# Kernel tuning notes

Hardware: AMD Instinct MI355X
Metric: run time of the kernel (lower is better)

## Reference

```python
import jax, jax.numpy as jnp
import numpy as np

T = 4096        # sequence length
D = 128         # input feature dim
TRACE = 64      # trace_size
CONTEXT = 64    # context_size
HID = 64        # internal dense width (hardcoded 64 in module)
OUT = 128       # output_size
LN_EPS = 1e-6   # flax LayerNorm default epsilon


def setup_inputs() -> dict:
    key = jax.random.key(0)
    ks = jax.random.split(key, 12)

    def dense(k, fi, fo):
        return (jax.random.normal(k, (fi, fo), jnp.float32) / np.sqrt(fi).astype(np.float32))

    inp = {}
    inp["x"] = jax.random.normal(ks[0], (T, D), jnp.float32)
    inp["state"] = jnp.zeros((1, TRACE, CONTEXT), jnp.complex64)
    inp["start"] = jax.random.uniform(ks[1], (T,)) < 0.01  # sparse episode resets
    # deterministic FFM decay / frequency params (init_deterministic)
    inp["a"] = jnp.linspace(1e-6, 0.5, TRACE).astype(jnp.float32)
    inp["b"] = (2.0 * jnp.pi / jnp.linspace(1.0, 1000.0, CONTEXT)).astype(jnp.float32)
    inp["W1"] = dense(ks[2], D, HID);               inp["b1"] = jnp.zeros((HID,), jnp.float32)
    inp["W2"] = dense(ks[3], HID, 2 * TRACE);       inp["b2"] = jnp.zeros((2 * TRACE,), jnp.float32)
    inp["Wgi"] = dense(ks[4], 2 * TRACE, TRACE);    inp["bgi"] = jnp.zeros((TRACE,), jnp.float32)
    inp["Wp"] = dense(ks[5], 2 * TRACE, TRACE);     inp["bp"] = jnp.zeros((TRACE,), jnp.float32)
    inp["Wz"] = dense(ks[6], 2 * TRACE * CONTEXT, HID); inp["bz"] = jnp.zeros((HID,), jnp.float32)
    inp["Wgo"] = dense(ks[7], 2 * TRACE, HID);      inp["bgo"] = jnp.zeros((HID,), jnp.float32)
    inp["Ws"] = dense(ks[8], 2 * TRACE, HID);       inp["bs"] = jnp.zeros((HID,), jnp.float32)
    inp["W3"] = dense(ks[9], HID, HID);             inp["b3"] = jnp.zeros((HID,), jnp.float32)
    inp["W4"] = dense(ks[10], HID, OUT);            inp["b4"] = jnp.zeros((OUT,), jnp.float32)
    return inp


def _ffm_scan(scan_in, state0, start, a, b):
    # scan_in: (T, TRACE, CONTEXT) float, state0: (1, TRACE, CONTEXT) complex64
    t = scan_in.shape[0]
    timestep = jnp.ones((t + 1, 1, 1), dtype=jnp.int32)
    start_f = jnp.concatenate(
        [jnp.zeros((1, 1, 1), dtype=bool), start.reshape(t, 1, 1)], axis=0)
    xs = jnp.concatenate([state0, scan_in.astype(jnp.complex64)], axis=0)

    neg_a = -jnp.abs(a).reshape(1, TRACE, 1)
    b_r = b.reshape(1, 1, CONTEXT)
    ab = neg_a + 1j * b_r  # (1, TRACE, CONTEXT) complex

    def gamma(j):
        # j: (N,1,1) int -> (N, TRACE, CONTEXT) complex decay
        return jnp.exp(ab * j.astype(jnp.float32))

    def combine(carry, incoming):
        prev_start, s, i = carry
        st, xx, j = incoming
        keep = jnp.logical_not(st)
        s = s * keep
        j = j * keep.astype(j.dtype)
        new_s = s * gamma(j) + xx
        return (jnp.logical_or(st, prev_start), new_s, j + i)

    _, new_state, _ = jax.lax.associative_scan(
        combine, (start_f, xs, timestep), axis=0)
    return new_state[1:]  # (T, TRACE, CONTEXT) complex64


def _layernorm(x):
    mu = jnp.mean(x, axis=-1, keepdims=True)
    var = jnp.var(x, axis=-1, keepdims=True)
    return (x - mu) * jax.lax.rsqrt(var + LN_EPS)


def _forward(x, state, start, a, b, W1, b1, W2, b2, Wgi, bgi, Wp, bp,
             Wz, bz, Wgo, bgo, Ws, bs, W3, b3, W4, b4):
    h = jax.nn.relu(x @ W1 + b1)                 # (T, 64)
    h2 = h @ W2 + b2                             # (T, 2*TRACE)
    gate_in = jax.nn.sigmoid(h2 @ Wgi + bgi)     # (T, TRACE)
    pre = jax.nn.sigmoid(h2 @ Wp + bp)           # (T, TRACE)
    gated = pre * gate_in                        # (T, TRACE)
    scan_in = jnp.broadcast_to(gated[:, :, None], (gated.shape[0], TRACE, CONTEXT))
    state_seq = _ffm_scan(scan_in, state, start, a, b)  # (T, TRACE, CONTEXT) c64
    z_in = jnp.concatenate([jnp.real(state_seq), jnp.imag(state_seq)],
                           axis=-1).reshape(state_seq.shape[0], -1)
    z = z_in @ Wz + bz                           # (T, 64)
    gate_out = jax.nn.sigmoid(h2 @ Wgo + bgo)    # (T, 64)
    skip = h2 @ Ws + bs                          # (T, 64)
    out = _layernorm(z * gate_out) + skip * (1.0 - gate_out)
    out = jax.nn.relu(out @ W3 + b3)
    out = out @ W4 + b4                          # (T, OUT)
    return out, state_seq[-1:]


def reference(x, state, start, a, b, W1, b1, W2, b2, Wgi, bgi, Wp, bp,
              Wz, bz, Wgo, bgo, Ws, bs, W3, b3, W4, b4):
    return _forward(x, state, start, a, b, W1, b1, W2, b2, Wgi, bgi, Wp, bp,
                    Wz, bz, Wgo, bgo, Ws, bs, W3, b3, W4, b4)
```

## Files before the change

kernel.cpp:

```cpp
#include <hip/hip_runtime.h>
#include <math.h>

#define T_LEN 4096
#define D_IN 128
#define HID 64
#define KDIM 4096
#define K2   8192

#define OFF_GATED 0u
#define OFF_GO    262144u
#define OFF_SKIP  524288u
#define OFF_PART  786432u
#define OFF_FLAGS 2883584u
#define OFF_CHS   2887680u
#define OFF_WZT   2887744u
#define OFF_STBF  3149888u

typedef __attribute__((ext_vector_type(8))) short short8v;
typedef __attribute__((ext_vector_type(4))) float float4v;

__device__ __forceinline__ float sigm(float x){ return 1.f/(1.f+expf(-x)); }
__device__ __forceinline__ unsigned short f2bf(float x){
    unsigned int u = __float_as_uint(x);
    return (unsigned short)((u + 0x7FFFu + ((u >> 16) & 1u)) >> 16);
}

__global__ __launch_bounds__(512) void k_prep(
    const unsigned char* __restrict__ su8, const int* __restrict__ si32,
    int* __restrict__ flags, int* __restrict__ chunkStart,
    const float* __restrict__ Wz, unsigned short* __restrict__ wzt,
    const float* __restrict__ x,
    const float* __restrict__ W1, const float* __restrict__ b1,
    const float* __restrict__ W2, const float* __restrict__ b2,
    const float* __restrict__ Wgi, const float* __restrict__ bgi,
    const float* __restrict__ Wp,  const float* __restrict__ bp,
    const float* __restrict__ Wgo, const float* __restrict__ bgo,
    const float* __restrict__ Wsk, const float* __restrict__ bsk,
    float* __restrict__ gated, float* __restrict__ go, float* __restrict__ sk)
{
    const int bx = blockIdx.x;
    const int tid = threadIdx.x;

    if (bx == 0) {
        __shared__ int cnt;
        if (tid == 0) cnt = 0;
        __syncthreads();
        int local = 0;
        for (int i = tid; i < 4096; i += 512)
            if (i & 3) local += su8[i];
        if (local) atomicAdd(&cnt, local);
        __syncthreads();
        if (cnt > 0) {
            for (int i = tid; i < 4096; i += 512) flags[i] = su8[i] ? 1 : 0;
        } else {
            for (int i = tid; i < 4096; i += 512) flags[i] = si32[i] ? 1 : 0;
        }
        __syncthreads();
        if (tid < 64) {
            int any = 0;
#pragma unroll 8
            for (int j = 0; j < 64; ++j) any |= flags[tid * 64 + j];
            chunkStart[tid] = any;
        }
        return;
    }
    if (bx <= 64) {
        int idx = ((bx - 1) * 512 + tid) * 16;
        int j = idx >> 13, k0 = idx & 8191;
#pragma unroll
        for (int e = 0; e < 16; ++e) {
            int k = k0 + e;
            int km = k & 4095;
            int m = km >> 6, c = km & 63;
            int row = m * 128 + ((k >= 4096) ? 64 : 0) + c;
            wzt[(size_t)j * K2 + k] = f2bf(Wz[(size_t)row * 64 + j]);
        }
        return;
    }

    __shared__ float xs[8][128];
    __shared__ float hs[8][64];
    __shared__ float h2s[8][128];
    __shared__ float tmp[8][4][64];
    const int t0 = (bx - 65) * 8;

    if (tid < 256) {
        int r = tid >> 5, kq = (tid & 31) << 2;
        *(float4*)&xs[r][kq] = *(const float4*)&x[(size_t)(t0 + r) * D_IN + kq];
    }

    const int j1 = tid >> 3, ks1 = tid & 7;
    float wr1[16];
#pragma unroll
    for (int kk = 0; kk < 16; ++kk) wr1[kk] = W1[(size_t)(ks1 * 16 + kk) * HID + j1];
    const float bias1 = b1[j1];
    __syncthreads();
#pragma unroll
    for (int r = 0; r < 8; ++r) {
        float p = 0.f;
#pragma unroll
        for (int kq = 0; kq < 4; ++kq) {
            float4 xv = *(const float4*)&xs[r][ks1 * 16 + kq * 4];
            p += xv.x * wr1[kq*4] + xv.y * wr1[kq*4+1] + xv.z * wr1[kq*4+2] + xv.w * wr1[kq*4+3];
        }
        p += __shfl_xor(p, 1, 64); p += __shfl_xor(p, 2, 64); p += __shfl_xor(p, 4, 64);
        if (ks1 == 0) hs[r][j1] = fmaxf(p + bias1, 0.f);
    }

    const int j2 = tid >> 2, ks2 = tid & 3;
    float wr2[16];
#pragma unroll
    for (int kk = 0; kk < 16; ++kk) wr2[kk] = W2[(size_t)(ks2 * 16 + kk) * 128 + j2];
    const float bias2 = b2[j2];
    __syncthreads();
#pragma unroll
    for (int r = 0; r < 8; ++r) {
        float p = 0.f;
#pragma unroll
        for (int kq = 0; kq < 4; ++kq) {
            float4 hv = *(const float4*)&hs[r][ks2 * 16 + kq * 4];
            p += hv.x * wr2[kq*4] + hv.y * wr2[kq*4+1] + hv.z * wr2[kq*4+2] + hv.w * wr2[kq*4+3];
        }
        p += __shfl_xor(p, 1, 64); p += __shfl_xor(p, 2, 64);
        if (ks2 == 0) h2s[r][j2] = p + bias2;
    }

    const int mat = tid >> 7, jj = (tid & 127) >> 1, kh = tid & 1;
    const float* Wm = (mat == 0) ? Wgi : (mat == 1) ? Wp : (mat == 2) ? Wgo : Wsk;
    float wgr[64];
#pragma unroll
    for (int kk = 0; kk < 64; ++kk) wgr[kk] = Wm[(size_t)(kh * 64 + kk) * 64 + jj];
    __syncthreads();
#pragma unroll
    for (int r = 0; r < 8; ++r) {
        float p = 0.f;
#pragma unroll
        for (int kq = 0; kq < 16; ++kq) {
            float4 hv = *(const float4*)&h2s[r][kh * 64 + kq * 4];
            p += hv.x * wgr[kq*4] + hv.y * wgr[kq*4+1] + hv.z * wgr[kq*4+2] + hv.w * wgr[kq*4+3];
        }
        p += __shfl_xor(p, 1, 64);
        if (kh == 0) tmp[r][mat][jj] = p;
    }
    __syncthreads();

    {
        int r = tid >> 6, j = tid & 63;
        int t = t0 + r;
        float gi = sigm(tmp[r][0][j] + bgi[j]);
        float pr = sigm(tmp[r][1][j] + bp[j]);
        float g  = sigm(tmp[r][2][j] + bgo[j]);
        float s  = tmp[r][3][j] + bsk[j];
        gated[t * 64 + j] = gi * pr;
        go[t * 64 + j]    = g;
        sk[t * 64 + j]    = s;
    }
}

__global__ __launch_bounds__(512) void k_scanA(
    const float* __restrict__ gated, const int* __restrict__ flags,
    const float* __restrict__ a, const float* __restrict__ b,
    float2* __restrict__ carryB)
{
    const int p = threadIdx.x >> 6, c = threadIdx.x & 63;
    const int pair = blockIdx.x * 8 + p;
    const int ch = pair & 63, m = pair >> 6;
    const int t0 = ch * 64;
    __shared__ float gb[8][64];
    __shared__ int fb[8][64];
    gb[p][c] = gated[(size_t)(t0 + c) * 64 + m];
    fb[p][c] = flags[t0 + c];
    __syncthreads();

    const double ea = exp(-fabs((double)a[m]));
    const double bb = (double)b[c];
    const double lre = ea * cos(bb), lim = ea * sin(bb);
    double sre = 0.0, sim = 0.0;
#pragma unroll 8
    for (int j = 0; j < 64; ++j) {
        double g = (double)gb[p][j];
        if (fb[p][j]) { sre = g; sim = 0.0; }
        else {
            double nr = fma(sre, lre, fma(-sim, lim, g));
            double ni = fma(sre, lim, sim * lre);
            sre = nr; sim = ni;
        }
    }
    carryB[(size_t)ch * KDIM + m * 64 + c] = make_float2((float)sre, (float)sim);
}

__global__ __launch_bounds__(64) void k_scanC(
    const float2* __restrict__ carryB, const int* __restrict__ chunkStart,
    const float* __restrict__ a, const float* __restrict__ b,
    const float* __restrict__ st0,
    float2* __restrict__ cinArr)
{
    const int m = blockIdx.x, c = threadIdx.x;
    __shared__ int chsS[64];
    chsS[c] = chunkStart[c];

    float2 Bv[64];
#pragma unroll
    for (int ch = 0; ch < 64; ++ch)
        Bv[ch] = carryB[(size_t)ch * KDIM + m * 64 + c];
    __syncthreads();

    const double ea64 = exp(-64.0 * fabs((double)a[m]));
    const double bb = (double)b[c];
    const double l64re = ea64 * cos(64.0 * bb), l64im = ea64 * sin(64.0 * bb);
    double cre = (double)st0[(m * 64 + c) * 2];
    double cim = (double)st0[(m * 64 + c) * 2 + 1];
#pragma unroll
    for (int ch = 0; ch < 64; ++ch) {
        cinArr[(size_t)ch * KDIM + m * 64 + c] = make_float2((float)cre, (float)cim);
        if (chsS[ch]) { cre = (double)Bv[ch].x; cim = (double)Bv[ch].y; }
        else {
            double nr = fma(cre, l64re, fma(-cim, l64im, (double)Bv[ch].x));
            double ni = fma(cre, l64im, fma(cim, l64re, (double)Bv[ch].y));
            cre = nr; cim = ni;
        }
    }
}

__global__ __launch_bounds__(512) void k_scanB(
    const float* __restrict__ gated, const int* __restrict__ flags,
    const float* __restrict__ a, const float* __restrict__ b,
    const float2* __restrict__ cinArr,
    unsigned short* __restrict__ stbf,
    float* __restrict__ out)
{
    const int p = threadIdx.x >> 6, c = threadIdx.x & 63;
    const int pair = blockIdx.x * 8 + p;
    const int ch = pair & 63, m = pair >> 6;
    const int t0 = ch * 64;
    __shared__ float gb[8][64];
    __shared__ int fb[8][64];
    gb[p][c] = gated[(size_t)(t0 + c) * 64 + m];
    fb[p][c] = flags[t0 + c];
    __syncthreads();

    const double ea = exp(-fabs((double)a[m]));
    const double bb = (double)b[c];
    const double lre = ea * cos(bb), lim = ea * sin(bb);
    float2 cin = cinArr[(size_t)ch * KDIM + m * 64 + c];
    double sre = (double)cin.x, sim = (double)cin.y;
#pragma unroll 4
    for (int j = 0; j < 64; ++j) {
        double g = (double)gb[p][j];
        if (fb[p][j]) { sre = g; sim = 0.0; }
        else {
            double nr = fma(sre, lre, fma(-sim, lim, g));
            double ni = fma(sre, lim, sim * lre);
            sre = nr; sim = ni;
        }
        unsigned short* strow = stbf + (size_t)(t0 + j) * K2;
        strow[m * 64 + c]        = f2bf((float)sre);
        strow[4096 + m * 64 + c] = f2bf((float)sim);
    }
    if (ch == 63) {
        out[524288 + m * 64 + c]        = (float)sre;
        out[524288 + 4096 + m * 64 + c] = (float)sim;
    }
}

__global__ __launch_bounds__(256) void k_zgemm(
    const unsigned short* __restrict__ stbf,
    const unsigned short* __restrict__ wzt,
    float* __restrict__ part)
{
    __shared__ char smem[65536];
    const int tid = threadIdx.x;
    const int w = tid >> 6, l = tid & 63;
    const int mb = blockIdx.x >> 3, kb = blockIdx.x & 7;
    const int kbase = kb * 1024;

    float4v acc[4];
#pragma unroll
    for (int i = 0; i < 4; ++i) acc[i] = (float4v){0.f, 0.f, 0.f, 0.f};

    for (int ks = 0; ks < 4; ++ks) {
#pragma unroll
        for (int it = 0; it < 8; ++it) {
            int ci = it * 256 + w * 64 + l;
            int r = ci >> 5, pc = ci & 31;
            int gc = pc ^ (r & 7);
            const unsigned short* gpA = stbf + (size_t)(mb * 64 + r) * K2 + kbase + ks * 256 + gc * 8;
            const unsigned short* gpB = wzt + (size_t)r * K2 + kbase + ks * 256 + gc * 8;
            char* lpA = smem + (it * 256 + w * 64) * 16;
            char* lpB = smem + 32768 + (it * 256 + w * 64) * 16;
            __builtin_amdgcn_global_load_lds(
                (const __attribute__((address_space(1))) void*)gpA,
                (__attribute__((address_space(3))) void*)lpA, 16, 0, 0);
            __builtin_amdgcn_global_load_lds(
                (const __attribute__((address_space(1))) void*)gpB,
                (__attribute__((address_space(3))) void*)lpB, 16, 0, 0);
        }
        __syncthreads();
        const int row_l = w * 16 + (l & 15);
        const int swz = (l & 7) << 4;
        const int ksub = (l >> 4) * 16;
#pragma unroll
        for (int k32 = 0; k32 < 8; ++k32) {
            int kbyte = k32 * 64 + ksub;
            short8v af = *(short8v*)(smem + row_l * 512 + (kbyte ^ swz));
#pragma unroll
            for (int nt = 0; nt < 4; ++nt) {
                int row_b = nt * 16 + (l & 15);
                short8v bf = *(short8v*)(smem + 32768 + row_b * 512 + (kbyte ^ swz));
                acc[nt] = __builtin_amdgcn_mfma_f32_16x16x32_bf16(af, bf, acc[nt], 0, 0, 0);
            }
        }
        __syncthreads();
    }

    float* pp = part + (size_t)kb * 262144;
    const int trow = mb * 64 + w * 16 + (l >> 4) * 4;
    const int jcol = l & 15;
#pragma unroll
    for (int nt = 0; nt < 4; ++nt)
#pragma unroll
        for (int r = 0; r < 4; ++r)
            pp[(size_t)(trow + r) * 64 + nt * 16 + jcol] = acc[nt][r];
}

__device__ __forceinline__ float wsum(float v) {
#pragma unroll
    for (int o = 32; o; o >>= 1) v += __shfl_xor(v, o, 64);
    return v;
}

__global__ __launch_bounds__(256) void k_epi(
    const float* __restrict__ part, const float* __restrict__ bz,
    const float* __restrict__ go, const float* __restrict__ sk,
    const float* __restrict__ W3, const float* __restrict__ b3,
    const float* __restrict__ W4, const float* __restrict__ b4,
    float* __restrict__ out)
{
    __shared__ float ob[4][64], hb[4][64];
    const int w = threadIdx.x >> 6, j = threadIdx.x & 63;
    const int t = blockIdx.x * 4 + w;
    float z = bz[j];
#pragma unroll
    for (int p = 0; p < 8; ++p) z += part[(size_t)p * 262144 + t * 64 + j];
    float g = go[t * 64 + j];
    float y = z * g;
    float mu = wsum(y) * 0.015625f;
    float d = y - mu;
    float var = wsum(d * d) * 0.015625f;
    float o = d * (1.f / sqrtf(var + 1e-6f)) + sk[t * 64 + j] * (1.f - g);
    ob[w][j] = o;
    __syncthreads();
    float acc = b3[j];
#pragma unroll 8
    for (int k = 0; k < 64; ++k) acc += ob[w][k] * W3[k * 64 + j];
    hb[w][j] = fmaxf(acc, 0.f);
    __syncthreads();
    float o1 = b4[j], o2 = b4[j + 64];
#pragma unroll 8
    for (int k = 0; k < 64; ++k) { float hv = hb[w][k]; o1 += hv * W4[k * 128 + j]; o2 += hv * W4[k * 128 + j + 64]; }
    out[(size_t)t * 128 + j] = o1;
    out[(size_t)t * 128 + j + 64] = o2;
}

extern "C" void kernel_launch(void* const* d_in, const int* in_sizes, int n_in,
                              void* d_out, int out_size, void* d_ws, size_t ws_size,
                              hipStream_t stream)
{
    const float* x   = (const float*)d_in[0];
    const float* st0 = (const float*)d_in[1];
    const void*  start = d_in[2];
    const float* a  = (const float*)d_in[3];
    const float* b  = (const float*)d_in[4];
    const float* W1 = (const float*)d_in[5];  const float* b1 = (const float*)d_in[6];
    const float* W2 = (const float*)d_in[7];  const float* b2 = (const float*)d_in[8];
    const float* Wgi= (const float*)d_in[9];  const float* bgi= (const float*)d_in[10];
    const float* Wp = (const float*)d_in[11]; const float* bp = (const float*)d_in[12];
    const float* Wz = (const float*)d_in[13]; const float* bz = (const float*)d_in[14];
    const float* Wgo= (const float*)d_in[15]; const float* bgo= (const float*)d_in[16];
    const float* Wsk= (const float*)d_in[17]; const float* bsk= (const float*)d_in[18];
    const float* W3 = (const float*)d_in[19]; const float* b3 = (const float*)d_in[20];
    const float* W4 = (const float*)d_in[21]; const float* b4 = (const float*)d_in[22];

    float* ws    = (float*)d_ws;
    float* out   = (float*)d_out;
    float* gated = ws + OFF_GATED;
    float* go    = ws + OFF_GO;
    float* sk    = ws + OFF_SKIP;
    float* part  = ws + OFF_PART;
    int*   flags = (int*)(ws + OFF_FLAGS);
    int*   chs   = (int*)(ws + OFF_CHS);
    unsigned short* wzt  = (unsigned short*)(ws + OFF_WZT);
    unsigned short* stbf = (unsigned short*)(ws + OFF_STBF);

    float2* carryB = (float2*)(part);
    float2* cinArr = (float2*)(part + 524288);

    hipLaunchKernelGGL(k_prep, dim3(577), dim3(512), 0, stream,
                       (const unsigned char*)start, (const int*)start, flags, chs,
                       Wz, wzt, x, W1, b1, W2, b2, Wgi, bgi, Wp, bp,
                       Wgo, bgo, Wsk, bsk, gated, go, sk);
    hipLaunchKernelGGL(k_scanA, dim3(512), dim3(512), 0, stream,
                       gated, flags, a, b, carryB);
    hipLaunchKernelGGL(k_scanC, dim3(64), dim3(64), 0, stream,
                       carryB, chs, a, b, st0, cinArr);
    hipLaunchKernelGGL(k_scanB, dim3(512), dim3(512), 0, stream,
                       gated, flags, a, b, cinArr, stbf, out);
    hipLaunchKernelGGL(k_zgemm, dim3(512), dim3(256), 0, stream, stbf, wzt, part);
    hipLaunchKernelGGL(k_epi, dim3(1024), dim3(256), 0, stream,
                       part, bz, go, sk, W3, b3, W4, b4, out);
}
```

Baseline: 92.19 us.

## Interleave re/im in state layout, stage scan output via LDS, double-buffer zgemm

Result: slower. 95.62 us (+3.7%).

```diff
diff --git a/kernel.cpp b/kernel.cpp
--- a/kernel.cpp
+++ b/kernel.cpp
@@ -70,10 +70,7 @@
 #pragma unroll
         for (int e = 0; e < 16; ++e) {
             int k = k0 + e;
-            int km = k & 4095;
-            int m = km >> 6, c = km & 63;
-            int row = m * 128 + ((k >= 4096) ? 64 : 0) + c;
-            wzt[(size_t)j * K2 + k] = f2bf(Wz[(size_t)row * 64 + j]);
+            wzt[(size_t)j * K2 + k] = f2bf(Wz[(size_t)k * 64 + j]);
         }
         return;
     }
@@ -222,21 +219,23 @@
     }
 }
 
-__global__ __launch_bounds__(512) void k_scanB(
+__global__ __launch_bounds__(256) void k_scanB(
     const float* __restrict__ gated, const int* __restrict__ flags,
     const float* __restrict__ a, const float* __restrict__ b,
     const float2* __restrict__ cinArr,
     unsigned short* __restrict__ stbf,
     float* __restrict__ out)
 {
-    const int p = threadIdx.x >> 6, c = threadIdx.x & 63;
-    const int pair = blockIdx.x * 8 + p;
-    const int ch = pair & 63, m = pair >> 6;
+    const int tid = threadIdx.x;
+    const int ml = tid >> 6, c = tid & 63;
+    const int ch = blockIdx.x & 63, mg = blockIdx.x >> 6;
+    const int m = mg * 4 + ml;
     const int t0 = ch * 64;
-    __shared__ float gb[8][64];
-    __shared__ int fb[8][64];
-    gb[p][c] = gated[(size_t)(t0 + c) * 64 + m];
-    fb[p][c] = flags[t0 + c];
+    __shared__ unsigned short st[64][512];
+    __shared__ float gb[4][64];
+    __shared__ int fb[64];
+    gb[ml][c] = gated[(size_t)(t0 + c) * 64 + m];
+    if (ml == 0) fb[c] = flags[t0 + c];
     __syncthreads();
 
     const double ea = exp(-fabs((double)a[m]));
@@ -246,16 +245,24 @@
     double sre = (double)cin.x, sim = (double)cin.y;
 #pragma unroll 4
     for (int j = 0; j < 64; ++j) {
-        double g = (double)gb[p][j];
-        if (fb[p][j]) { sre = g; sim = 0.0; }
+        double g = (double)gb[ml][j];
+        if (fb[j]) { sre = g; sim = 0.0; }
         else {
             double nr = fma(sre, lre, fma(-sim, lim, g));
             double ni = fma(sre, lim, sim * lre);
             sre = nr; sim = ni;
         }
-        unsigned short* strow = stbf + (size_t)(t0 + j) * K2;
-        strow[m * 64 + c]        = f2bf((float)sre);
-        strow[4096 + m * 64 + c] = f2bf((float)sim);
+        st[j][ml * 128 + c]      = f2bf((float)sre);
+        st[j][ml * 128 + 64 + c] = f2bf((float)sim);
+    }
+    __syncthreads();
+
+#pragma unroll
+    for (int it = 0; it < 16; ++it) {
+        int idx = it * 256 + tid;
+        int row = idx >> 6, colB = (idx & 63) * 16;
+        *(uint4*)((char*)(stbf + (size_t)(t0 + row) * K2 + mg * 512) + colB) =
+            *(const uint4*)((const char*)st + row * 1024 + colB);
     }
     if (ch == 63) {
         out[524288 + m * 64 + c]        = (float)sre;
@@ -278,40 +285,47 @@
 #pragma unroll
     for (int i = 0; i < 4; ++i) acc[i] = (float4v){0.f, 0.f, 0.f, 0.f};
 
-    for (int ks = 0; ks < 4; ++ks) {
-#pragma unroll
-        for (int it = 0; it < 8; ++it) {
-            int ci = it * 256 + w * 64 + l;
-            int r = ci >> 5, pc = ci & 31;
-            int gc = pc ^ (r & 7);
-            const unsigned short* gpA = stbf + (size_t)(mb * 64 + r) * K2 + kbase + ks * 256 + gc * 8;
-            const unsigned short* gpB = wzt + (size_t)r * K2 + kbase + ks * 256 + gc * 8;
-            char* lpA = smem + (it * 256 + w * 64) * 16;
-            char* lpB = smem + 32768 + (it * 256 + w * 64) * 16;
-            __builtin_amdgcn_global_load_lds(
-                (const __attribute__((address_space(1))) void*)gpA,
-                (__attribute__((address_space(3))) void*)lpA, 16, 0, 0);
-            __builtin_amdgcn_global_load_lds(
-                (const __attribute__((address_space(1))) void*)gpB,
-                (__attribute__((address_space(3))) void*)lpB, 16, 0, 0);
-        }
-        __syncthreads();
-        const int row_l = w * 16 + (l & 15);
-        const int swz = (l & 7) << 4;
-        const int ksub = (l >> 4) * 16;
-#pragma unroll
-        for (int k32 = 0; k32 < 8; ++k32) {
+#define ZSTAGE(s, d)                                                                              \
+    _Pragma("unroll")                                                                             \
+    for (int it = 0; it < 4; ++it) {                                                              \
+        int ci = it * 256 + tid;                                                                  \
+        int r = ci >> 4, pc = ci & 15;                                                            \
+        int gc = pc ^ (r & 7);                                                                    \
+        const unsigned short* gpA = stbf + (size_t)(mb * 64 + r) * K2 + kbase + (s) * 128 + gc * 8;\
+        const unsigned short* gpB = wzt + (size_t)r * K2 + kbase + (s) * 128 + gc * 8;            \
+        __builtin_amdgcn_global_load_lds(                                                         \
+            (const __attribute__((address_space(1))) void*)gpA,                                   \
+            (__attribute__((address_space(3))) void*)(smem + (d) * 32768 + ci * 16), 16, 0, 0);   \
+        __builtin_amdgcn_global_load_lds(                                                         \
+            (const __attribute__((address_space(1))) void*)gpB,                                   \
+            (__attribute__((address_space(3))) void*)(smem + (d) * 32768 + 16384 + ci * 16), 16, 0, 0); \
+    }
+
+    ZSTAGE(0, 0);
+    __syncthreads();
+    const int row_l = w * 16 + (l & 15);
+    const int swz = (l & 7) << 4;
+    const int ksub = (l >> 4) * 16;
+#pragma unroll
+    for (int s = 0; s < 8; ++s) {
+        const int cur = s & 1;
+        if (s < 7) { ZSTAGE(s + 1, cur ^ 1); }
+        const char* bufA = smem + cur * 32768;
+        const char* bufB = bufA + 16384;
+#pragma unroll
+        for (int k32 = 0; k32 < 4; ++k32) {
             int kbyte = k32 * 64 + ksub;
-            short8v af = *(short8v*)(smem + row_l * 512 + (kbyte ^ swz));
+            short8v af = *(const short8v*)(bufA + row_l * 256 + (kbyte ^ swz));
 #pragma unroll
             for (int nt = 0; nt < 4; ++nt) {
                 int row_b = nt * 16 + (l & 15);
-                short8v bf = *(short8v*)(smem + 32768 + row_b * 512 + (kbyte ^ swz));
+                short8v bf = *(const short8v*)(bufB + row_b * 256 + (kbyte ^ swz));
                 acc[nt] = __builtin_amdgcn_mfma_f32_16x16x32_bf16(af, bf, acc[nt], 0, 0, 0);
             }
         }
         __syncthreads();
     }
+#undef ZSTAGE
 
     float* pp = part + (size_t)kb * 262144;
     const int trow = mb * 64 + w * 16 + (l >> 4) * 4;
@@ -403,7 +417,7 @@
                        gated, flags, a, b, carryB);
     hipLaunchKernelGGL(k_scanC, dim3(64), dim3(64), 0, stream,
                        carryB, chs, a, b, st0, cinArr);
-    hipLaunchKernelGGL(k_scanB, dim3(512), dim3(512), 0, stream,
+    hipLaunchKernelGGL(k_scanB, dim3(1024), dim3(256), 0, stream,
                        gated, flags, a, b, cinArr, stbf, out);
     hipLaunchKernelGGL(k_zgemm, dim3(512), dim3(256), 0, stream, stbf, wzt, part);
     hipLaunchKernelGGL(k_epi, dim3(1024), dim3(256), 0, stream,
```
